# Kernel tuning notes

Measured on AMD Instinct MI355X. Metric: run time of the kernel, lower is better.

## Reference

```python
import jax, jax.numpy as jnp
import numpy as np

HIDDEN = 1024
H = 16        # num query heads
HKV = 4       # num kv heads
GROUPS = H // HKV
D = HIDDEN // H  # head_dim = 64
SW = (63, 0)  # sliding_window (left, right)
W = SW[0] + SW[1] + 1  # window length per query = 64
MAXPOS = 2048


def _sincos_table(num_pos, dim):
    # faithful to create_sinusoidal_positions (incl. final [:, :, :num_pos] slice)
    inv_freq = 1.0 / 10000 ** (np.arange(0, dim, 2, dtype=np.int32) / dim)
    freqs = np.einsum('i,j->ij', np.arange(num_pos, dtype=np.int32), inv_freq).astype(np.float32)
    emb = np.concatenate((freqs, freqs), axis=-1)
    out = np.concatenate((np.sin(emb)[:, None, :], np.cos(emb)[:, None, :]), axis=-1)
    return jnp.asarray(out[:, :, :num_pos])  # [num_pos, 1, 2*dim]

_SINCOS = _sincos_table(MAXPOS, D)


def _rotate_half(x):
    h = x.shape[-1] // 2
    return jnp.concatenate((-x[..., h:], x[..., :h]), axis=-1)


def setup_inputs() -> dict:
    key = jax.random.key(0)
    k0, k1, k2, k3, k4 = jax.random.split(key, 5)
    B, S = 1, 2048
    std = 0.02
    return {
        'hidden_states': jax.random.normal(k0, (B, S, HIDDEN), dtype=jnp.float32),
        'attention_mask': jnp.ones((B, S, 1, W), dtype=jnp.int32),
        'position_ids': jnp.arange(B * S, dtype=jnp.int32).reshape(B, S) % MAXPOS,
        'q_kernel': jax.random.normal(k1, (HIDDEN, H * D), dtype=jnp.float32) * std,
        'k_kernel': jax.random.normal(k2, (HIDDEN, HKV * D), dtype=jnp.float32) * std,
        'v_kernel': jax.random.normal(k3, (HIDDEN, HKV * D), dtype=jnp.float32) * std,
        'o_kernel': jax.random.normal(k4, (HIDDEN, HIDDEN), dtype=jnp.float32) * std,
    }


def reference(hidden_states, attention_mask, position_ids, q_kernel, k_kernel, v_kernel, o_kernel):
    B, S, _ = hidden_states.shape
    # QKV projections (no bias)
    q = (hidden_states @ q_kernel).reshape(B, S, H, D)
    k = (hidden_states @ k_kernel).reshape(B, S, HKV, D)
    v = (hidden_states @ v_kernel).reshape(B, S, HKV, D)
    # rotary embedding; sincos[pos] -> [B,S,1,2D], broadcasts over head axis
    sc = _SINCOS[position_ids]
    sin, cos = jnp.split(sc, 2, axis=-1)
    k = k * cos + _rotate_half(k) * sin
    q = q * cos + _rotate_half(q) * sin
    # GQA: repeat kv heads to match query heads
    k = jnp.repeat(k, GROUPS, axis=2)  # [B,S,H,D]
    v = jnp.repeat(v, GROUPS, axis=2)
    # sliding-window gather: each query position sees W surrounding keys
    k = jnp.pad(k, ((0, 0), SW, (0, 0), (0, 0)))
    v = jnp.pad(v, ((0, 0), SW, (0, 0), (0, 0)))
    idx = jnp.arange(W, dtype=jnp.int32)[None, :] + jnp.arange(S, dtype=jnp.int32)[:, None]  # [S,W]
    kg = k[:, idx]  # [B,S,W,H,D]
    vg = v[:, idx]
    # attention (q_len=1 per position), scores [B,S,H,W]
    scores = jnp.einsum('bshd,bswhd->bshw', q, kg) / jnp.asarray(np.sqrt(D), scores_dtype := jnp.float32)
    neg = jnp.finfo(jnp.float32).min
    m = attention_mask[:, :, 0, :][:, :, None, :]  # [B,S,1,W] broadcast over H
    bias = jnp.where(m > 0, jnp.float32(0.0), neg)
    weights = jax.nn.softmax(scores + bias, axis=-1)
    attn = jnp.einsum('bshw,bswhd->bshd', weights, vg).reshape(B, S, HIDDEN)
    return attn @ o_kernel
```

## Files before the change

kernel.cpp:

```cpp
#include <hip/hip_runtime.h>
#include <hip/hip_bf16.h>
#include <math.h>

#define S        2048
#define HIDDEN   1024
#define NH       16
#define NKV      4
#define HD       64
#define NQKV     1536

typedef _Float16 f16x8 __attribute__((ext_vector_type(8)));
typedef _Float16 f16x4 __attribute__((ext_vector_type(4)));
typedef float    f32x4 __attribute__((ext_vector_type(4)));

__device__ __forceinline__ void glds16(const void* g, void* l) {
    __builtin_amdgcn_global_load_lds((const __attribute__((address_space(1))) void*)g,
                                     (__attribute__((address_space(3))) void*)l, 16, 0, 0);
}

__global__ __launch_bounds__(256) void prep_kernel(const float* __restrict__ hs, _Float16* __restrict__ hsf16,
                                                   const float* __restrict__ wq, const float* __restrict__ wk,
                                                   const float* __restrict__ wvv, const float* __restrict__ wo,
                                                   _Float16* __restrict__ wqkvT, _Float16* __restrict__ woT) {
    int bid = blockIdx.x;
    int tid = threadIdx.x;
    if (bid >= 2560) {
        int i = (bid - 2560) * 256 + tid;
        float4 v = ((const float4*)hs)[i];
        f16x4 o = { (_Float16)v.x, (_Float16)v.y, (_Float16)v.z, (_Float16)v.w };
        *(f16x4*)(hsf16 + 4 * (size_t)i) = o;
        return;
    }
    const float* src; _Float16* dst; int Cn, b;
    if (bid < 1024)      { src = wq;  dst = wqkvT;                       Cn = 1024; b = bid; }
    else if (bid < 1280) { src = wk;  dst = wqkvT + (size_t)1024 * 1024; Cn = 256;  b = bid - 1024; }
    else if (bid < 1536) { src = wvv; dst = wqkvT + (size_t)1280 * 1024; Cn = 256;  b = bid - 1280; }
    else                 { src = wo;  dst = woT;                         Cn = 1024; b = bid - 1536; }
    int xb = Cn >> 5;
    int c0 = (b % xb) * 32;
    int r0 = (b / xb) * 32;
    __shared__ float t[32][33];
    int tx = tid & 31, ty = tid >> 5;
#pragma unroll
    for (int i = ty; i < 32; i += 8)
        t[i][tx] = src[(size_t)(r0 + i) * Cn + c0 + tx];
    __syncthreads();
#pragma unroll
    for (int i = ty; i < 32; i += 8)
        dst[(size_t)(c0 + i) * 1024 + r0 + tx] = (_Float16)t[tx][i];
}

template <typename OutT>
__global__ __launch_bounds__(256) void gemm_glds(const _Float16* __restrict__ A,
                                                 const _Float16* __restrict__ BT,
                                                 OutT* __restrict__ C,
                                                 int M, int N, int K) {
    const int m0   = blockIdx.y * 128;
    const int n0   = blockIdx.x * 64;
    const int tid  = threadIdx.x;
    const int lane = tid & 63;
    const int wv   = tid >> 6;
    const int lr   = lane & 15;
    const int quad = lane >> 4;
    const int wm   = (wv >> 1) * 64;
    const int wn   = (wv & 1) * 32;
    const int dr   = lane >> 3;
    const int cc   = lane & 7;

    __shared__ __align__(16) _Float16 As[128 * 64];
    __shared__ __align__(16) _Float16 Bs[64 * 64];

    f32x4 acc[4][2] = {};

    for (int k0 = 0; k0 < K; k0 += 64) {
        __syncthreads();
#pragma unroll
        for (int t = 0; t < 4; ++t) {
            int r = wv * 32 + t * 8 + dr;
            glds16(A + (size_t)(m0 + r) * K + k0 + (cc ^ (r & 7)) * 8,
                   As + (wv * 32 + t * 8) * 64);
        }
#pragma unroll
        for (int t = 0; t < 2; ++t) {
            int r = wv * 16 + t * 8 + dr;
            glds16(BT + (size_t)(n0 + r) * K + k0 + (cc ^ (r & 7)) * 8,
                   Bs + (wv * 16 + t * 8) * 64);
        }
        __syncthreads();
#pragma unroll
        for (int k8 = 0; k8 < 8; k8 += 4) {
            f16x8 a[4], b[2];
#pragma unroll
            for (int i = 0; i < 4; ++i) {
                int row = wm + i * 16 + lr;
                a[i] = *(const f16x8*)&As[row * 64 + ((quad + k8) ^ (row & 7)) * 8];
            }
#pragma unroll
            for (int j = 0; j < 2; ++j) {
                int row = wn + j * 16 + lr;
                b[j] = *(const f16x8*)&Bs[row * 64 + ((quad + k8) ^ (row & 7)) * 8];
            }
#pragma unroll
            for (int i = 0; i < 4; ++i)
#pragma unroll
                for (int j = 0; j < 2; ++j)
                    acc[i][j] = __builtin_amdgcn_mfma_f32_16x16x32_f16(a[i], b[j], acc[i][j], 0, 0, 0);
        }
    }
#pragma unroll
    for (int i = 0; i < 4; ++i)
#pragma unroll
        for (int j = 0; j < 2; ++j)
#pragma unroll
            for (int r = 0; r < 4; ++r)
                C[(size_t)(m0 + wm + i * 16 + quad * 4 + r) * N + n0 + wn + j * 16 + lr] = (OutT)acc[i][j][r];
}

__global__ __launch_bounds__(256) void attn_mfma(const _Float16* __restrict__ qkv,
                                                 const int* __restrict__ mask,
                                                 const int* __restrict__ pos_ids,
                                                 _Float16* __restrict__ attn_out) {
    const int s0   = blockIdx.x * 16;
    const int g    = blockIdx.y;
    const int tid  = threadIdx.x;
    const int lane = tid & 63;
    const int wv   = tid >> 6;
    const int h    = g * 4 + wv;
    const int lr   = lane & 15;
    const int quad = lane >> 4;

    __shared__ __align__(16) _Float16 K_lds[80 * 72];
    __shared__ __align__(16) _Float16 Vt_lds[64 * 104];
    __shared__ __align__(16) _Float16 P_lds[4][16 * 104];
    __shared__ int M_lds[1024];
    __shared__ double invf[32];

    ((int4*)M_lds)[tid] = ((const int4*)(mask + s0 * 64))[tid];
    if (tid < 32) invf[tid] = pow(10000.0, -(double)(2 * tid) / 64.0);
    __syncthreads();

    for (int c = tid; c < 320; c += 256) {
        int r = c >> 2, cl = c & 3;
        int j = s0 - 63 + r;
        f16x8 nlo = {}, nhi = {};
        if (j >= 0 && r < 79) {
            f16x8 lo = *(const f16x8*)(qkv + (size_t)j * NQKV + 1024 + g * 64 + cl * 8);
            f16x8 hi = *(const f16x8*)(qkv + (size_t)j * NQKV + 1024 + g * 64 + 32 + cl * 8);
            int pos = pos_ids[j];
#pragma unroll
            for (int e = 0; e < 8; ++e) {
                float ang = (float)((double)pos * invf[cl * 8 + e]);
                float sn, cs;
                sincosf(ang, &sn, &cs);
                float x1 = (float)lo[e], x2 = (float)hi[e];
                nlo[e] = (_Float16)(x1 * cs - x2 * sn);
                nhi[e] = (_Float16)(x2 * cs + x1 * sn);
            }
        }
        *(f16x8*)&K_lds[r * 72 + cl * 8]       = nlo;
        *(f16x8*)&K_lds[r * 72 + (cl + 4) * 8] = nhi;
    }
    for (int c = tid; c < 96 * 8; c += 256) {
        int r = c >> 3, cl = c & 7;
        int j = s0 - 63 + r;
        f16x8 val = {};
        if (j >= 0 && r < 79)
            val = *(const f16x8*)(qkv + (size_t)j * NQKV + 1280 + g * 64 + cl * 8);
#pragma unroll
        for (int d8 = 0; d8 < 8; ++d8)
            Vt_lds[(cl * 8 + d8) * 104 + r] = val[d8];
    }

    f16x8 qf[2];
    {
        int posq = pos_ids[s0 + lr];
        f16x8 q0 = *(const f16x8*)(qkv + (size_t)(s0 + lr) * NQKV + h * 64 + quad * 8);
        f16x8 q1 = *(const f16x8*)(qkv + (size_t)(s0 + lr) * NQKV + h * 64 + 32 + quad * 8);
        f16x8 n0, n1;
#pragma unroll
        for (int e = 0; e < 8; ++e) {
            float ang = (float)((double)posq * invf[quad * 8 + e]);
            float sn, cs;
            sincosf(ang, &sn, &cs);
            float x1 = (float)q0[e], x2 = (float)q1[e];
            n0[e] = (_Float16)((x1 * cs - x2 * sn) * 0.125f);
            n1[e] = (_Float16)((x2 * cs + x1 * sn) * 0.125f);
        }
        qf[0] = n0; qf[1] = n1;
    }
    __syncthreads();

    f32x4 sc[5];
#pragma unroll
    for (int t = 0; t < 5; ++t) {
        f32x4 a = {};
#pragma unroll
        for (int ks = 0; ks < 2; ++ks) {
            f16x8 kf = *(const f16x8*)&K_lds[(t * 16 + lr) * 72 + ks * 32 + quad * 8];
            a = __builtin_amdgcn_mfma_f32_16x16x32_f16(qf[ks], kf, a, 0, 0, 0);
        }
        sc[t] = a;
    }

#pragma unroll
    for (int t = 0; t < 5; ++t)
#pragma unroll
        for (int r = 0; r < 4; ++r) {
            int qi = quad * 4 + r;
            int w  = t * 16 + lr - qi;
            bool ok = (w >= 0) && (w < 64) && (M_lds[qi * 64 + (w & 63)] > 0);
            sc[t][r] = ok ? sc[t][r] : -1e30f;
        }

    float pr[5][4];
#pragma unroll
    for (int r = 0; r < 4; ++r) {
        float mx = -1e30f;
#pragma unroll
        for (int t = 0; t < 5; ++t) mx = fmaxf(mx, sc[t][r]);
#pragma unroll
        for (int off = 1; off < 16; off <<= 1) mx = fmaxf(mx, __shfl_xor(mx, off));
        float sum = 0.f;
#pragma unroll
        for (int t = 0; t < 5; ++t) { float e = __expf(sc[t][r] - mx); pr[t][r] = e; sum += e; }
#pragma unroll
        for (int off = 1; off < 16; off <<= 1) sum += __shfl_xor(sum, off);
        float rs = 1.0f / sum;
#pragma unroll
        for (int t = 0; t < 5; ++t) pr[t][r] *= rs;
    }

    _Float16* myP = P_lds[wv];
    {
        f16x4 z = {};
        *(f16x4*)&myP[lr * 104 + 80 + quad * 4] = z;
    }
#pragma unroll
    for (int t = 0; t < 5; ++t)
#pragma unroll
        for (int r = 0; r < 4; ++r)
            myP[(quad * 4 + r) * 104 + t * 16 + lr] = (_Float16)pr[t][r];
    __syncthreads();

    f32x4 oacc[4] = {};
#pragma unroll
    for (int ks = 0; ks < 3; ++ks) {
        f16x8 pf = *(const f16x8*)&myP[lr * 104 + ks * 32 + quad * 8];
#pragma unroll
        for (int t = 0; t < 4; ++t) {
            f16x8 vf = *(const f16x8*)&Vt_lds[(t * 16 + lr) * 104 + ks * 32 + quad * 8];
            oacc[t] = __builtin_amdgcn_mfma_f32_16x16x32_f16(pf, vf, oacc[t], 0, 0, 0);
        }
    }
#pragma unroll
    for (int t = 0; t < 4; ++t)
#pragma unroll
        for (int r = 0; r < 4; ++r)
            attn_out[(size_t)(s0 + quad * 4 + r) * HIDDEN + h * 64 + t * 16 + lr] = (_Float16)oacc[t][r];
}

extern "C" void kernel_launch(void* const* d_in, const int* in_sizes, int n_in,
                              void* d_out, int out_size, void* d_ws, size_t ws_size,
                              hipStream_t stream) {
    const float* hs      = (const float*)d_in[0];
    const int*   mask    = (const int*)  d_in[1];
    const int*   pos_ids = (const int*)  d_in[2];
    const float* wq      = (const float*)d_in[3];
    const float* wk      = (const float*)d_in[4];
    const float* wvv     = (const float*)d_in[5];
    const float* wo      = (const float*)d_in[6];
    float* out = (float*)d_out;

    char* ws = (char*)d_ws;
    _Float16* hsf16   = (_Float16*)(ws + 0);
    _Float16* wqkvT   = (_Float16*)(ws + (4u << 20));
    _Float16* woT     = (_Float16*)(ws + (7u << 20));
    _Float16* qkvf16  = (_Float16*)(ws + (9u << 20));
    _Float16* attnf16 = (_Float16*)(ws + (15u << 20));

    prep_kernel<<<4608, 256, 0, stream>>>(hs, hsf16, wq, wk, wvv, wo, wqkvT, woT);
    gemm_glds<_Float16><<<dim3(NQKV / 64, S / 128), 256, 0, stream>>>(hsf16, wqkvT, qkvf16, S, NQKV, HIDDEN);
    attn_mfma<<<dim3(S / 16, NKV), 256, 0, stream>>>(qkvf16, mask, pos_ids, attnf16);
    gemm_glds<float><<<dim3(HIDDEN / 64, S / 128), 256, 0, stream>>>(attnf16, woT, out, S, HIDDEN, HIDDEN);
}
```

Baseline: 123.7 us.

## Fuse hidden-state f16 cast into QKV GEMM and double-buffer GEMM tiles

Drops the separate fp32-to-f16 conversion of hidden_states from the prep kernel; the QKV GEMM now loads fp32 A and converts it while staging into LDS. Both GEMMs switch from direct global-to-LDS loads with a swizzle to a register-staged, double-buffered pipeline that prefetches the next K tile during the MFMAs, with one barrier per iteration. This removes a pass over the activations and hides load latency, but it uses more registers and LDS and drops the XOR swizzle, which may bring back LDS bank conflicts.

```diff
diff --git a/kernel.cpp b/kernel.cpp
--- a/kernel.cpp
+++ b/kernel.cpp
@@ -13,24 +13,11 @@
 typedef _Float16 f16x4 __attribute__((ext_vector_type(4)));
 typedef float    f32x4 __attribute__((ext_vector_type(4)));
 
-__device__ __forceinline__ void glds16(const void* g, void* l) {
-    __builtin_amdgcn_global_load_lds((const __attribute__((address_space(1))) void*)g,
-                                     (__attribute__((address_space(3))) void*)l, 16, 0, 0);
-}
-
-__global__ __launch_bounds__(256) void prep_kernel(const float* __restrict__ hs, _Float16* __restrict__ hsf16,
-                                                   const float* __restrict__ wq, const float* __restrict__ wk,
+__global__ __launch_bounds__(256) void prep_kernel(const float* __restrict__ wq, const float* __restrict__ wk,
                                                    const float* __restrict__ wvv, const float* __restrict__ wo,
                                                    _Float16* __restrict__ wqkvT, _Float16* __restrict__ woT) {
     int bid = blockIdx.x;
     int tid = threadIdx.x;
-    if (bid >= 2560) {
-        int i = (bid - 2560) * 256 + tid;
-        float4 v = ((const float4*)hs)[i];
-        f16x4 o = { (_Float16)v.x, (_Float16)v.y, (_Float16)v.z, (_Float16)v.w };
-        *(f16x4*)(hsf16 + 4 * (size_t)i) = o;
-        return;
-    }
     const float* src; _Float16* dst; int Cn, b;
     if (bid < 1024)      { src = wq;  dst = wqkvT;                       Cn = 1024; b = bid; }
     else if (bid < 1280) { src = wk;  dst = wqkvT + (size_t)1024 * 1024; Cn = 256;  b = bid - 1024; }
@@ -50,11 +37,13 @@
         dst[(size_t)(c0 + i) * 1024 + r0 + tx] = (_Float16)t[tx][i];
 }
 
-template <typename OutT>
-__global__ __launch_bounds__(256) void gemm_glds(const _Float16* __restrict__ A,
+template <bool F32A, typename OutT>
+__global__ __launch_bounds__(256) void gemm_pipe(const void* __restrict__ Avoid,
                                                  const _Float16* __restrict__ BT,
                                                  OutT* __restrict__ C,
                                                  int M, int N, int K) {
+    const float*    Af = (const float*)Avoid;
+    const _Float16* Ah = (const _Float16*)Avoid;
     const int m0   = blockIdx.y * 128;
     const int n0   = blockIdx.x * 64;
     const int tid  = threadIdx.x;
@@ -64,49 +53,106 @@
     const int quad = lane >> 4;
     const int wm   = (wv >> 1) * 64;
     const int wn   = (wv & 1) * 32;
-    const int dr   = lane >> 3;
-    const int cc   = lane & 7;
-
-    __shared__ __align__(16) _Float16 As[128 * 64];
-    __shared__ __align__(16) _Float16 Bs[64 * 64];
+
+    __shared__ __align__(16) _Float16 As[2][128 * 64];
+    __shared__ __align__(16) _Float16 Bs[2][64 * 64];
+
+    const int ar8 = tid >> 3, ac8 = tid & 7;
+    const int ar4 = tid >> 4, ac4 = tid & 15;
 
     f32x4 acc[4][2] = {};
-
-    for (int k0 = 0; k0 < K; k0 += 64) {
-        __syncthreads();
-#pragma unroll
-        for (int t = 0; t < 4; ++t) {
-            int r = wv * 32 + t * 8 + dr;
-            glds16(A + (size_t)(m0 + r) * K + k0 + (cc ^ (r & 7)) * 8,
-                   As + (wv * 32 + t * 8) * 64);
-        }
-#pragma unroll
-        for (int t = 0; t < 2; ++t) {
-            int r = wv * 16 + t * 8 + dr;
-            glds16(BT + (size_t)(n0 + r) * K + k0 + (cc ^ (r & 7)) * 8,
-                   Bs + (wv * 16 + t * 8) * 64);
-        }
-        __syncthreads();
-#pragma unroll
-        for (int k8 = 0; k8 < 8; k8 += 4) {
+    float4 aRf[8];
+    uint4  aRh[4];
+    uint4  bR[2];
+
+    if (F32A) {
+#pragma unroll
+        for (int i = 0; i < 8; ++i) {
+            int r = ar4 + i * 16;
+            float4 v = *(const float4*)(Af + (size_t)(m0 + r) * K + ac4 * 4);
+            f16x4 h = { (_Float16)v.x, (_Float16)v.y, (_Float16)v.z, (_Float16)v.w };
+            *(f16x4*)&As[0][r * 64 + ac4 * 4] = h;
+        }
+    } else {
+#pragma unroll
+        for (int i = 0; i < 4; ++i) {
+            int r = ar8 + i * 32;
+            *(uint4*)&As[0][r * 64 + ac8 * 8] = *(const uint4*)(Ah + (size_t)(m0 + r) * K + ac8 * 8);
+        }
+    }
+#pragma unroll
+    for (int i = 0; i < 2; ++i) {
+        int r = ar8 + i * 32;
+        *(uint4*)&Bs[0][r * 64 + ac8 * 8] = *(const uint4*)(BT + (size_t)(n0 + r) * K + ac8 * 8);
+    }
+    __syncthreads();
+
+    int p = 0;
+    for (int k0 = 64; k0 < K; k0 += 64) {
+        if (F32A) {
+#pragma unroll
+            for (int i = 0; i < 8; ++i)
+                aRf[i] = *(const float4*)(Af + (size_t)(m0 + ar4 + i * 16) * K + k0 + ac4 * 4);
+        } else {
+#pragma unroll
+            for (int i = 0; i < 4; ++i)
+                aRh[i] = *(const uint4*)(Ah + (size_t)(m0 + ar8 + i * 32) * K + k0 + ac8 * 8);
+        }
+#pragma unroll
+        for (int i = 0; i < 2; ++i)
+            bR[i] = *(const uint4*)(BT + (size_t)(n0 + ar8 + i * 32) * K + k0 + ac8 * 8);
+
+#pragma unroll
+        for (int ks = 0; ks < 2; ++ks) {
             f16x8 a[4], b[2];
 #pragma unroll
-            for (int i = 0; i < 4; ++i) {
-                int row = wm + i * 16 + lr;
-                a[i] = *(const f16x8*)&As[row * 64 + ((quad + k8) ^ (row & 7)) * 8];
-            }
-#pragma unroll
-            for (int j = 0; j < 2; ++j) {
-                int row = wn + j * 16 + lr;
-                b[j] = *(const f16x8*)&Bs[row * 64 + ((quad + k8) ^ (row & 7)) * 8];
-            }
+            for (int i = 0; i < 4; ++i)
+                a[i] = *(const f16x8*)&As[p][(wm + i * 16 + lr) * 64 + (ks * 4 + quad) * 8];
+#pragma unroll
+            for (int j = 0; j < 2; ++j)
+                b[j] = *(const f16x8*)&Bs[p][(wn + j * 16 + lr) * 64 + (ks * 4 + quad) * 8];
 #pragma unroll
             for (int i = 0; i < 4; ++i)
 #pragma unroll
                 for (int j = 0; j < 2; ++j)
                     acc[i][j] = __builtin_amdgcn_mfma_f32_16x16x32_f16(a[i], b[j], acc[i][j], 0, 0, 0);
         }
-    }
+
+        if (F32A) {
+#pragma unroll
+            for (int i = 0; i < 8; ++i) {
+                float4 v = aRf[i];
+                f16x4 h = { (_Float16)v.x, (_Float16)v.y, (_Float16)v.z, (_Float16)v.w };
+                *(f16x4*)&As[p ^ 1][(ar4 + i * 16) * 64 + ac4 * 4] = h;
+            }
+        } else {
+#pragma unroll
+            for (int i = 0; i < 4; ++i)
+                *(uint4*)&As[p ^ 1][(ar8 + i * 32) * 64 + ac8 * 8] = aRh[i];
+        }
+#pragma unroll
+        for (int i = 0; i < 2; ++i)
+            *(uint4*)&Bs[p ^ 1][(ar8 + i * 32) * 64 + ac8 * 8] = bR[i];
+        __syncthreads();
+        p ^= 1;
+    }
+
+#pragma unroll
+    for (int ks = 0; ks < 2; ++ks) {
+        f16x8 a[4], b[2];
+#pragma unroll
+        for (int i = 0; i < 4; ++i)
+            a[i] = *(const f16x8*)&As[p][(wm + i * 16 + lr) * 64 + (ks * 4 + quad) * 8];
+#pragma unroll
+        for (int j = 0; j < 2; ++j)
+            b[j] = *(const f16x8*)&Bs[p][(wn + j * 16 + lr) * 64 + (ks * 4 + quad) * 8];
+#pragma unroll
+        for (int i = 0; i < 4; ++i)
+#pragma unroll
+            for (int j = 0; j < 2; ++j)
+                acc[i][j] = __builtin_amdgcn_mfma_f32_16x16x32_f16(a[i], b[j], acc[i][j], 0, 0, 0);
+    }
+
 #pragma unroll
     for (int i = 0; i < 4; ++i)
 #pragma unroll
@@ -272,14 +318,13 @@
     float* out = (float*)d_out;
 
     char* ws = (char*)d_ws;
-    _Float16* hsf16   = (_Float16*)(ws + 0);
-    _Float16* wqkvT   = (_Float16*)(ws + (4u << 20));
-    _Float16* woT     = (_Float16*)(ws + (7u << 20));
-    _Float16* qkvf16  = (_Float16*)(ws + (9u << 20));
-    _Float16* attnf16 = (_Float16*)(ws + (15u << 20));
-
-    prep_kernel<<<4608, 256, 0, stream>>>(hs, hsf16, wq, wk, wvv, wo, wqkvT, woT);
-    gemm_glds<_Float16><<<dim3(NQKV / 64, S / 128), 256, 0, stream>>>(hsf16, wqkvT, qkvf16, S, NQKV, HIDDEN);
+    _Float16* wqkvT   = (_Float16*)(ws + 0);
+    _Float16* woT     = (_Float16*)(ws + (3u << 20));
+    _Float16* qkvf16  = (_Float16*)(ws + (5u << 20));
+    _Float16* attnf16 = (_Float16*)(ws + (11u << 20));
+
+    prep_kernel<<<2560, 256, 0, stream>>>(wq, wk, wvv, wo, wqkvT, woT);
+    gemm_pipe<true, _Float16><<<dim3(NQKV / 64, S / 128), 256, 0, stream>>>(hs, wqkvT, qkvf16, S, NQKV, HIDDEN);
     attn_mfma<<<dim3(S / 16, NKV), 256, 0, stream>>>(qkvf16, mask, pos_ids, attnf16);
-    gemm_glds<float><<<dim3(HIDDEN / 64, S / 128), 256, 0, stream>>>(attnf16, woT, out, S, HIDDEN, HIDDEN);
+    gemm_pipe<false, float><<<dim3(HIDDEN / 64, S / 128), 256, 0, stream>>>(attnf16, woT, out, S, HIDDEN, HIDDEN);
 }
```

Result: slower. 128.4 us (+3.7%).
